# Performance work log

Measured on AMD Instinct MI355X. Metric: run time of the kernel, lower is better.

## Reference

```python
import jax, jax.numpy as jnp
import numpy as np

B = 512          # batch of visual features
VF_D = 4096      # visual feature dim (VGG fc7)
HID_D = 2048     # hidden dim
EMB_D = 300      # order-embedding / label-vector dim
N_LABELS = 2000  # number of GT label vectors


def setup_inputs() -> dict:
    key = jax.random.key(0)
    ks = jax.random.split(key, 4)
    vfs = jax.random.normal(ks[0], (B, VF_D), dtype=jnp.float32)
    W1 = jax.random.normal(ks[1], (VF_D, HID_D), dtype=jnp.float32) * (1.0 / np.sqrt(VF_D))
    b1 = jnp.zeros((HID_D,), dtype=jnp.float32)
    W2 = jax.random.normal(ks[2], (HID_D, EMB_D), dtype=jnp.float32) * (1.0 / np.sqrt(HID_D))
    b2 = jnp.zeros((EMB_D,), dtype=jnp.float32)
    gt_label_vecs = jax.random.normal(ks[3], (N_LABELS, EMB_D), dtype=jnp.float32)
    return {"vfs": vfs, "W1": W1, "b1": b1, "W2": W2, "b2": b2,
            "gt_label_vecs": gt_label_vecs}


def reference(vfs, W1, b1, W2, b2, gt_label_vecs):
    # hidden_layer: ReLU -> (Dropout, identity at eval) -> Linear
    vf_hidden = jnp.dot(jax.nn.relu(vfs), W1) + b1            # [B, HID_D]
    # embedding_layer: ReLU -> Linear
    vf_emb = jnp.dot(jax.nn.relu(vf_hidden), W2) + b2         # [B, EMB_D]
    # order_sim(hypers=gt_label_vecs, hypos=vf_emb):
    #   score = -|| clamp(hypo - hyper, min=0) ||^2, batched over all pairs
    diff = jax.nn.relu(vf_emb[:, None, :] - gt_label_vecs[None, :, :])  # [B, N, D]
    score_stack = -jnp.sum(diff * diff, axis=-1)              # [B, N_LABELS]
    return score_stack, vf_emb
```

## Files before the change

### kernel.cpp

```cpp
#include <hip/hip_runtime.h>

#define B_SZ   512
#define VFD    4096
#define HIDD   2048
#define EMBD   300
#define NLAB   2000
#define NPAD   320

typedef __attribute__((ext_vector_type(8))) short short8x;
typedef __attribute__((ext_vector_type(4))) float f32x4;
typedef __attribute__((ext_vector_type(8))) unsigned short ushort8;
typedef __attribute__((ext_vector_type(4))) unsigned short ushort4x;

typedef const __attribute__((address_space(1))) unsigned int* gas_t;
typedef __attribute__((address_space(3))) unsigned int* las_t;

__device__ inline unsigned short f2bf(float x) {
    unsigned u = __float_as_uint(x);
    u += 0x7FFF + ((u >> 16) & 1);
    return (unsigned short)(u >> 16);
}

__global__ __launch_bounds__(256) void conv_relu_bf16_kernel(
    const float* __restrict__ in, unsigned short* __restrict__ out)
{
    const int i = (blockIdx.x * 256 + threadIdx.x) * 8;
    float4 a = *(const float4*)&in[i];
    float4 b = *(const float4*)&in[i + 4];
    ushort8 o;
    o[0] = f2bf(fmaxf(a.x, 0.f)); o[1] = f2bf(fmaxf(a.y, 0.f));
    o[2] = f2bf(fmaxf(a.z, 0.f)); o[3] = f2bf(fmaxf(a.w, 0.f));
    o[4] = f2bf(fmaxf(b.x, 0.f)); o[5] = f2bf(fmaxf(b.y, 0.f));
    o[6] = f2bf(fmaxf(b.z, 0.f)); o[7] = f2bf(fmaxf(b.w, 0.f));
    *(ushort8*)&out[i] = o;
}

__global__ __launch_bounds__(256) void transpose_conv_kernel(
    const float* __restrict__ in, unsigned short* __restrict__ out,
    int N, int ldK)
{
    __shared__ float tile[64][65];
    const int tid = threadIdx.x;
    const int n0 = blockIdx.x * 64, k0 = blockIdx.y * 64;

    #pragma unroll
    for (int i = 0; i < 4; ++i) {
        const int s = tid + 256 * i;
        const int kr = s >> 4, nc = (s & 15) * 4;
        float4 v = {0.f, 0.f, 0.f, 0.f};
        if (n0 + nc < N) v = *(const float4*)&in[(size_t)(k0 + kr) * N + n0 + nc];
        tile[kr][nc + 0] = v.x; tile[kr][nc + 1] = v.y;
        tile[kr][nc + 2] = v.z; tile[kr][nc + 3] = v.w;
    }
    __syncthreads();

    const int row = tid >> 2, kq = (tid & 3) * 16;
    ushort8 o0, o1;
    #pragma unroll
    for (int j = 0; j < 8; ++j) o0[j] = f2bf(tile[kq + j][row]);
    #pragma unroll
    for (int j = 0; j < 8; ++j) o1[j] = f2bf(tile[kq + 8 + j][row]);
    const size_t off = (size_t)(n0 + row) * ldK + k0 + kq;
    *(ushort8*)&out[off]     = o0;
    *(ushort8*)&out[off + 8] = o1;
}

template<int LDA, int LDB, int LDC, int KCHUNK>
__global__ __launch_bounds__(256) void gemm_bf16_kernel(
    const unsigned short* __restrict__ A,
    const unsigned short* __restrict__ Bt,
    float* __restrict__ Cpart, int M)
{
    __shared__ unsigned short As[2048];
    __shared__ unsigned short Bs[2048];

    const int tid = threadIdx.x;
    const int m0 = blockIdx.y * 64, n0 = blockIdx.x * 64;
    const int kbase = blockIdx.z * KCHUNK;

    const int soct = tid >> 6, srow = tid & 63;
    const unsigned short* ga = A  + (size_t)(m0 + srow) * LDA + kbase + soct * 8;
    const unsigned short* gb = Bt + (size_t)(n0 + srow) * LDB + kbase + soct * 8;
    las_t la = (las_t)(void*)&As[tid * 8];
    las_t lb = (las_t)(void*)&Bs[tid * 8];

    const int lane = tid & 63;
    const int wave = tid >> 6;
    const int wm = (wave & 1) * 32;
    const int wn = (wave >> 1) * 32;
    const int q = lane >> 4, l15 = lane & 15;

    f32x4 acc00 = {0.f,0.f,0.f,0.f}, acc01 = {0.f,0.f,0.f,0.f};
    f32x4 acc10 = {0.f,0.f,0.f,0.f}, acc11 = {0.f,0.f,0.f,0.f};

    const int iters = KCHUNK / 32;
    for (int t = 0; t < iters; ++t) {
        __builtin_amdgcn_global_load_lds((gas_t)(const void*)(ga + t * 32), la, 16, 0, 0);
        __builtin_amdgcn_global_load_lds((gas_t)(const void*)(gb + t * 32), lb, 16, 0, 0);
        __syncthreads();

        short8x a0 = *(short8x*)&As[(q * 64 + wm +      l15) * 8];
        short8x a1 = *(short8x*)&As[(q * 64 + wm + 16 + l15) * 8];
        short8x b0 = *(short8x*)&Bs[(q * 64 + wn +      l15) * 8];
        short8x b1 = *(short8x*)&Bs[(q * 64 + wn + 16 + l15) * 8];
        acc00 = __builtin_amdgcn_mfma_f32_16x16x32_bf16(a0, b0, acc00, 0, 0, 0);
        acc01 = __builtin_amdgcn_mfma_f32_16x16x32_bf16(a0, b1, acc01, 0, 0, 0);
        acc10 = __builtin_amdgcn_mfma_f32_16x16x32_bf16(a1, b0, acc10, 0, 0, 0);
        acc11 = __builtin_amdgcn_mfma_f32_16x16x32_bf16(a1, b1, acc11, 0, 0, 0);
        __syncthreads();
    }

    float* Cz = Cpart + (size_t)blockIdx.z * M * LDC;
    #pragma unroll
    for (int r = 0; r < 4; ++r) {
        const int rr = m0 + wm + q * 4 + r;
        const int cc = n0 + wn + l15;
        Cz[(size_t)rr * LDC + cc]             = acc00[r];
        Cz[(size_t)rr * LDC + cc + 16]        = acc01[r];
        Cz[(size_t)(rr + 16) * LDC + cc]      = acc10[r];
        Cz[(size_t)(rr + 16) * LDC + cc + 16] = acc11[r];
    }
}

__global__ __launch_bounds__(256) void reduce_h_kernel(
    const float* __restrict__ Hpart, const float* __restrict__ b1,
    unsigned short* __restrict__ Hb)
{
    const int i = (blockIdx.x * 256 + threadIdx.x) * 4;
    const int col = i & (HIDD - 1);
    float4 p0 = *(const float4*)&Hpart[i];
    float4 p1 = *(const float4*)&Hpart[(size_t)B_SZ * HIDD + i];
    float4 bb = *(const float4*)&b1[col];
    ushort4x o;
    o[0] = f2bf(fmaxf(p0.x + p1.x + bb.x, 0.f));
    o[1] = f2bf(fmaxf(p0.y + p1.y + bb.y, 0.f));
    o[2] = f2bf(fmaxf(p0.z + p1.z + bb.z, 0.f));
    o[3] = f2bf(fmaxf(p0.w + p1.w + bb.w, 0.f));
    *(ushort4x*)&Hb[i] = o;
}

__global__ __launch_bounds__(256) void reduce_e_kernel(
    const float* __restrict__ Epart, const float* __restrict__ b2,
    float* __restrict__ E)
{
    const int gid = blockIdx.x * 256 + threadIdx.x;
    if (gid >= B_SZ * EMBD) return;
    const int m = gid / EMBD, n = gid - m * EMBD;
    float v = b2[n];
    #pragma unroll
    for (int z = 0; z < 4; ++z)
        v += Epart[(size_t)z * B_SZ * NPAD + m * NPAD + n];
    E[gid] = v;
}

__global__ __launch_bounds__(256) void scores_kernel(
    const float* __restrict__ E, const float* __restrict__ G,
    float* __restrict__ out)
{
    __shared__ float Es[32][68];
    __shared__ float Gs[64][68];

    const int tid = threadIdx.x;
    const int tx = tid & 15, ty = tid >> 4;
    const int n0 = blockIdx.x * 64, b0 = blockIdx.y * 32;

    float acc[2][4] = {};

    for (int dc = 0; dc < 320; dc += 64) {
        #pragma unroll
        for (int i = 0; i < 2; ++i) {
            const int s = tid + 256 * i;
            const int row = s >> 4, qd = (s & 15) * 4;
            const int d = dc + qd;
            float4 v = {0.f, 0.f, 0.f, 0.f};
            if (d < EMBD) v = *(const float4*)&E[(size_t)(b0 + row) * EMBD + d];
            *(float4*)&Es[row][qd] = v;
        }
        #pragma unroll
        for (int i = 0; i < 4; ++i) {
            const int s = tid + 256 * i;
            const int row = s >> 4, qd = (s & 15) * 4;
            const int d = dc + qd;
            const int n = n0 + row;
            float4 v = {0.f, 0.f, 0.f, 0.f};
            if (n < NLAB && d < EMBD) v = *(const float4*)&G[(size_t)n * EMBD + d];
            *(float4*)&Gs[row][qd] = v;
        }
        __syncthreads();

        #pragma unroll 4
        for (int d = 0; d < 64; d += 4) {
            float4 e0 = *(float4*)&Es[ty * 2][d];
            float4 e1 = *(float4*)&Es[ty * 2 + 1][d];
            #pragma unroll
            for (int r = 0; r < 4; ++r) {
                float4 g = *(float4*)&Gs[tx + 16 * r][d];
                float t0;
                t0 = fmaxf(e0.x - g.x, 0.f); acc[0][r] += t0 * t0;
                t0 = fmaxf(e0.y - g.y, 0.f); acc[0][r] += t0 * t0;
                t0 = fmaxf(e0.z - g.z, 0.f); acc[0][r] += t0 * t0;
                t0 = fmaxf(e0.w - g.w, 0.f); acc[0][r] += t0 * t0;
                t0 = fmaxf(e1.x - g.x, 0.f); acc[1][r] += t0 * t0;
                t0 = fmaxf(e1.y - g.y, 0.f); acc[1][r] += t0 * t0;
                t0 = fmaxf(e1.z - g.z, 0.f); acc[1][r] += t0 * t0;
                t0 = fmaxf(e1.w - g.w, 0.f); acc[1][r] += t0 * t0;
            }
        }
        __syncthreads();
    }

    #pragma unroll
    for (int p = 0; p < 2; ++p) {
        const int b = b0 + ty * 2 + p;
        #pragma unroll
        for (int r = 0; r < 4; ++r) {
            const int n = n0 + tx + 16 * r;
            if (n < NLAB) out[(size_t)b * NLAB + n] = -acc[p][r];
        }
    }
}

extern "C" void kernel_launch(void* const* d_in, const int* in_sizes, int n_in,
                              void* d_out, int out_size, void* d_ws, size_t ws_size,
                              hipStream_t stream)
{
    const float* vfs = (const float*)d_in[0];
    const float* W1  = (const float*)d_in[1];
    const float* b1  = (const float*)d_in[2];
    const float* W2  = (const float*)d_in[3];
    const float* b2  = (const float*)d_in[4];
    const float* G   = (const float*)d_in[5];

    float* out    = (float*)d_out;
    float* scores = out;
    float* E      = out + (size_t)B_SZ * NLAB;

    char* ws = (char*)d_ws;
    unsigned short* Xb  = (unsigned short*)(ws);
    unsigned short* W1T = (unsigned short*)(ws + 4194304);
    unsigned short* W2T = (unsigned short*)(ws + 20971520);
    unsigned short* Hb  = (unsigned short*)(ws + 22282240);
    float*          Hpart = (float*)(ws + 24379392);
    float*          Epart = (float*)(ws + 32768000);

    conv_relu_bf16_kernel<<<1024, 256, 0, stream>>>(vfs, Xb);
    transpose_conv_kernel<<<dim3(32, 64), 256, 0, stream>>>(W1, W1T, HIDD, VFD);
    transpose_conv_kernel<<<dim3(5, 32), 256, 0, stream>>>(W2, W2T, EMBD, HIDD);

    gemm_bf16_kernel<VFD, VFD, HIDD, 2048>
        <<<dim3(32, 8, 2), 256, 0, stream>>>(Xb, W1T, Hpart, B_SZ);
    reduce_h_kernel<<<1024, 256, 0, stream>>>(Hpart, b1, Hb);

    gemm_bf16_kernel<HIDD, HIDD, NPAD, 512>
        <<<dim3(5, 8, 4), 256, 0, stream>>>(Hb, W2T, Epart, B_SZ);
    reduce_e_kernel<<<600, 256, 0, stream>>>(Epart, b2, E);

    scores_kernel<<<dim3(32, 16), 256, 0, stream>>>(E, G, scores);
}
```

Measured before the change: 180.4 us.

## Double-buffer GEMM LDS tiles, fuse prep kernels, and raise split-K factors

Merges the ReLU/convert and two weight transpose kernels into a single launch dispatched by block index. The bf16 GEMM now uses two LDS buffers, prefetching the next K-slice while computing the current one, and drops one barrier per iteration. Split-K is increased to 4 for the first GEMM and 8 for the second to launch more blocks, at the cost of more partial-sum traffic in the reduce kernels.

```diff
diff --git a/kernel.cpp b/kernel.cpp
--- a/kernel.cpp
+++ b/kernel.cpp
@@ -7,6 +7,9 @@
 #define NLAB   2000
 #define NPAD   320
 
+#define G1_SPLIT 4
+#define G2_SPLIT 8
+
 typedef __attribute__((ext_vector_type(8))) short short8x;
 typedef __attribute__((ext_vector_type(4))) float f32x4;
 typedef __attribute__((ext_vector_type(8))) unsigned short ushort8;
@@ -21,27 +24,37 @@
     return (unsigned short)(u >> 16);
 }
 
-__global__ __launch_bounds__(256) void conv_relu_bf16_kernel(
-    const float* __restrict__ in, unsigned short* __restrict__ out)
-{
-    const int i = (blockIdx.x * 256 + threadIdx.x) * 8;
-    float4 a = *(const float4*)&in[i];
-    float4 b = *(const float4*)&in[i + 4];
-    ushort8 o;
-    o[0] = f2bf(fmaxf(a.x, 0.f)); o[1] = f2bf(fmaxf(a.y, 0.f));
-    o[2] = f2bf(fmaxf(a.z, 0.f)); o[3] = f2bf(fmaxf(a.w, 0.f));
-    o[4] = f2bf(fmaxf(b.x, 0.f)); o[5] = f2bf(fmaxf(b.y, 0.f));
-    o[6] = f2bf(fmaxf(b.z, 0.f)); o[7] = f2bf(fmaxf(b.w, 0.f));
-    *(ushort8*)&out[i] = o;
-}
-
-__global__ __launch_bounds__(256) void transpose_conv_kernel(
-    const float* __restrict__ in, unsigned short* __restrict__ out,
-    int N, int ldK)
+__global__ __launch_bounds__(256) void prep_kernel(
+    const float* __restrict__ vfs, unsigned short* __restrict__ Xb,
+    const float* __restrict__ W1, unsigned short* __restrict__ W1T,
+    const float* __restrict__ W2, unsigned short* __restrict__ W2T)
 {
     __shared__ float tile[64][65];
     const int tid = threadIdx.x;
-    const int n0 = blockIdx.x * 64, k0 = blockIdx.y * 64;
+    const int blk = blockIdx.x;
+
+    if (blk < 1024) {
+        const int i = (blk * 256 + tid) * 8;
+        float4 a = *(const float4*)&vfs[i];
+        float4 b = *(const float4*)&vfs[i + 4];
+        ushort8 o;
+        o[0] = f2bf(fmaxf(a.x, 0.f)); o[1] = f2bf(fmaxf(a.y, 0.f));
+        o[2] = f2bf(fmaxf(a.z, 0.f)); o[3] = f2bf(fmaxf(a.w, 0.f));
+        o[4] = f2bf(fmaxf(b.x, 0.f)); o[5] = f2bf(fmaxf(b.y, 0.f));
+        o[6] = f2bf(fmaxf(b.z, 0.f)); o[7] = f2bf(fmaxf(b.w, 0.f));
+        *(ushort8*)&Xb[i] = o;
+        return;
+    }
+
+    const float* in; unsigned short* out; int N, ldK, bx, by;
+    if (blk < 3072) {
+        const int b = blk - 1024;
+        in = W1; out = W1T; N = HIDD; ldK = VFD; bx = b & 31; by = b >> 5;
+    } else {
+        const int b = blk - 3072;
+        in = W2; out = W2T; N = EMBD; ldK = HIDD; bx = b % 5; by = b / 5;
+    }
+    const int n0 = bx * 64, k0 = by * 64;
 
     #pragma unroll
     for (int i = 0; i < 4; ++i) {
@@ -71,8 +84,8 @@
     const unsigned short* __restrict__ Bt,
     float* __restrict__ Cpart, int M)
 {
-    __shared__ unsigned short As[2048];
-    __shared__ unsigned short Bs[2048];
+    __shared__ unsigned short As[2][2048];
+    __shared__ unsigned short Bs[2][2048];
 
     const int tid = threadIdx.x;
     const int m0 = blockIdx.y * 64, n0 = blockIdx.x * 64;
@@ -81,8 +94,6 @@
     const int soct = tid >> 6, srow = tid & 63;
     const unsigned short* ga = A  + (size_t)(m0 + srow) * LDA + kbase + soct * 8;
     const unsigned short* gb = Bt + (size_t)(n0 + srow) * LDB + kbase + soct * 8;
-    las_t la = (las_t)(void*)&As[tid * 8];
-    las_t lb = (las_t)(void*)&Bs[tid * 8];
 
     const int lane = tid & 63;
     const int wave = tid >> 6;
@@ -93,21 +104,31 @@
     f32x4 acc00 = {0.f,0.f,0.f,0.f}, acc01 = {0.f,0.f,0.f,0.f};
     f32x4 acc10 = {0.f,0.f,0.f,0.f}, acc11 = {0.f,0.f,0.f,0.f};
 
+    __builtin_amdgcn_global_load_lds((gas_t)(const void*)ga,
+                                     (las_t)(void*)&As[0][tid * 8], 16, 0, 0);
+    __builtin_amdgcn_global_load_lds((gas_t)(const void*)gb,
+                                     (las_t)(void*)&Bs[0][tid * 8], 16, 0, 0);
+
     const int iters = KCHUNK / 32;
     for (int t = 0; t < iters; ++t) {
-        __builtin_amdgcn_global_load_lds((gas_t)(const void*)(ga + t * 32), la, 16, 0, 0);
-        __builtin_amdgcn_global_load_lds((gas_t)(const void*)(gb + t * 32), lb, 16, 0, 0);
+        const int cur = t & 1, nxt = cur ^ 1;
         __syncthreads();
 
-        short8x a0 = *(short8x*)&As[(q * 64 + wm +      l15) * 8];
-        short8x a1 = *(short8x*)&As[(q * 64 + wm + 16 + l15) * 8];
-        short8x b0 = *(short8x*)&Bs[(q * 64 + wn +      l15) * 8];
-        short8x b1 = *(short8x*)&Bs[(q * 64 + wn + 16 + l15) * 8];
+        if (t + 1 < iters) {
+            __builtin_amdgcn_global_load_lds((gas_t)(const void*)(ga + (t + 1) * 32),
+                                             (las_t)(void*)&As[nxt][tid * 8], 16, 0, 0);
+            __builtin_amdgcn_global_load_lds((gas_t)(const void*)(gb + (t + 1) * 32),
+                                             (las_t)(void*)&Bs[nxt][tid * 8], 16, 0, 0);
+        }
+
+        short8x a0 = *(short8x*)&As[cur][(q * 64 + wm +      l15) * 8];
+        short8x a1 = *(short8x*)&As[cur][(q * 64 + wm + 16 + l15) * 8];
+        short8x b0 = *(short8x*)&Bs[cur][(q * 64 + wn +      l15) * 8];
+        short8x b1 = *(short8x*)&Bs[cur][(q * 64 + wn + 16 + l15) * 8];
         acc00 = __builtin_amdgcn_mfma_f32_16x16x32_bf16(a0, b0, acc00, 0, 0, 0);
         acc01 = __builtin_amdgcn_mfma_f32_16x16x32_bf16(a0, b1, acc01, 0, 0, 0);
         acc10 = __builtin_amdgcn_mfma_f32_16x16x32_bf16(a1, b0, acc10, 0, 0, 0);
         acc11 = __builtin_amdgcn_mfma_f32_16x16x32_bf16(a1, b1, acc11, 0, 0, 0);
-        __syncthreads();
     }
 
     float* Cz = Cpart + (size_t)blockIdx.z * M * LDC;
@@ -128,14 +149,17 @@
 {
     const int i = (blockIdx.x * 256 + threadIdx.x) * 4;
     const int col = i & (HIDD - 1);
-    float4 p0 = *(const float4*)&Hpart[i];
-    float4 p1 = *(const float4*)&Hpart[(size_t)B_SZ * HIDD + i];
-    float4 bb = *(const float4*)&b1[col];
+    float4 s = *(const float4*)&b1[col];
+    #pragma unroll
+    for (int z = 0; z < G1_SPLIT; ++z) {
+        float4 p = *(const float4*)&Hpart[(size_t)z * B_SZ * HIDD + i];
+        s.x += p.x; s.y += p.y; s.z += p.z; s.w += p.w;
+    }
     ushort4x o;
-    o[0] = f2bf(fmaxf(p0.x + p1.x + bb.x, 0.f));
-    o[1] = f2bf(fmaxf(p0.y + p1.y + bb.y, 0.f));
-    o[2] = f2bf(fmaxf(p0.z + p1.z + bb.z, 0.f));
-    o[3] = f2bf(fmaxf(p0.w + p1.w + bb.w, 0.f));
+    o[0] = f2bf(fmaxf(s.x, 0.f));
+    o[1] = f2bf(fmaxf(s.y, 0.f));
+    o[2] = f2bf(fmaxf(s.z, 0.f));
+    o[3] = f2bf(fmaxf(s.w, 0.f));
     *(ushort4x*)&Hb[i] = o;
 }
 
@@ -148,7 +172,7 @@
     const int m = gid / EMBD, n = gid - m * EMBD;
     float v = b2[n];
     #pragma unroll
-    for (int z = 0; z < 4; ++z)
+    for (int z = 0; z < G2_SPLIT; ++z)
         v += Epart[(size_t)z * B_SZ * NPAD + m * NPAD + n];
     E[gid] = v;
 }
@@ -241,18 +265,16 @@
     unsigned short* W2T = (unsigned short*)(ws + 20971520);
     unsigned short* Hb  = (unsigned short*)(ws + 22282240);
     float*          Hpart = (float*)(ws + 24379392);
-    float*          Epart = (float*)(ws + 32768000);
-
-    conv_relu_bf16_kernel<<<1024, 256, 0, stream>>>(vfs, Xb);
-    transpose_conv_kernel<<<dim3(32, 64), 256, 0, stream>>>(W1, W1T, HIDD, VFD);
-    transpose_conv_kernel<<<dim3(5, 32), 256, 0, stream>>>(W2, W2T, EMBD, HIDD);
-
-    gemm_bf16_kernel<VFD, VFD, HIDD, 2048>
-        <<<dim3(32, 8, 2), 256, 0, stream>>>(Xb, W1T, Hpart, B_SZ);
+    float*          Epart = (float*)(ws + 41156608);
+
+    prep_kernel<<<3232, 256, 0, stream>>>(vfs, Xb, W1, W1T, W2, W2T);
+
+    gemm_bf16_kernel<VFD, VFD, HIDD, VFD / G1_SPLIT>
+        <<<dim3(32, 8, G1_SPLIT), 256, 0, stream>>>(Xb, W1T, Hpart, B_SZ);
     reduce_h_kernel<<<1024, 256, 0, stream>>>(Hpart, b1, Hb);
 
-    gemm_bf16_kernel<HIDD, HIDD, NPAD, 512>
-        <<<dim3(5, 8, 4), 256, 0, stream>>>(Hb, W2T, Epart, B_SZ);
+    gemm_bf16_kernel<HIDD, HIDD, NPAD, HIDD / G2_SPLIT>
+        <<<dim3(5, 8, G2_SPLIT), 256, 0, stream>>>(Hb, W2T, Epart, B_SZ);
     reduce_e_kernel<<<600, 256, 0, stream>>>(Epart, b2, E);
 
     scores_kernel<<<dim3(32, 16), 256, 0, stream>>>(E, G, scores);
```

Measured after the change: 173.5 us. -3.8%, faster.
